# Kernel tuning notes

Measured on AMD Instinct MI355X. Metric: run time of the kernel, lower is better.

Reference implementation:

```python
import jax, jax.numpy as jnp
import numpy as np

DIM = 2048
NH = 16
Q_LORA = 1536
KV_LORA = 512
NOPE = 128
ROPE = 64
VDIM = 128
QK = NOPE + ROPE  # 192
B, S = 2, 2048
EPS = 1.1920929e-07  # torch.finfo(float32).eps (nn.RMSNorm default)


def linear(x, w, b):
    return jnp.einsum('...i,oi->...o', x, w) + b


def rmsnorm(x, w):
    ms = jnp.mean(x * x, axis=-1, keepdims=True)
    return x * jax.lax.rsqrt(ms + EPS) * w


def rope(x, cos, sin):
    # x: [B,S,H,d] interleaved pairs; cos/sin: [S, d//2]
    x = x.reshape(*x.shape[:-1], -1, 2)
    x0, x1 = x[..., 0], x[..., 1]
    c = cos[None, :, None, :]
    s = sin[None, :, None, :]
    y0 = x0 * c - x1 * s
    y1 = x0 * s + x1 * c
    return jnp.stack([y0, y1], axis=-1).reshape(*x.shape[:-2], -1)


def setup_inputs() -> dict:
    key = jax.random.key(0)
    ks = jax.random.split(key, 12)
    sd = 0.02
    x = jax.random.normal(ks[0], (B, S, DIM), dtype=jnp.float32)
    freqs = jax.random.normal(ks[1], (S, ROPE // 2), dtype=jnp.float32)
    causal_mask = jnp.where(jnp.triu(jnp.ones((S, S), bool), k=1), -1e9, 0.0).astype(jnp.float32)
    inp = dict(x=x, freqs=freqs, causal_mask=causal_mask)
    inp['Wq_down_w'] = sd * jax.random.normal(ks[2], (Q_LORA, DIM), dtype=jnp.float32)
    inp['Wq_down_b'] = jnp.zeros((Q_LORA,), jnp.float32)
    inp['q_norm_w'] = jnp.ones((Q_LORA,), jnp.float32)
    inp['Wq_up_w'] = sd * jax.random.normal(ks[3], (NH * QK, Q_LORA), dtype=jnp.float32)
    inp['Wq_up_b'] = jnp.zeros((NH * QK,), jnp.float32)
    inp['Wkv_down_w'] = sd * jax.random.normal(ks[4], (KV_LORA + ROPE, DIM), dtype=jnp.float32)
    inp['Wkv_down_b'] = jnp.zeros((KV_LORA + ROPE,), jnp.float32)
    inp['kv_norm_w'] = jnp.ones((KV_LORA,), jnp.float32)
    inp['Wkv_up_w'] = sd * jax.random.normal(ks[5], (NH * (NOPE + VDIM), KV_LORA), dtype=jnp.float32)
    inp['Wkv_up_b'] = jnp.zeros((NH * (NOPE + VDIM),), jnp.float32)
    inp['Wo_w'] = sd * jax.random.normal(ks[6], (DIM, NH * VDIM), dtype=jnp.float32)
    inp['Wo_b'] = jnp.zeros((DIM,), jnp.float32)
    return inp


def reference(x, freqs, causal_mask, Wq_down_w, Wq_down_b, q_norm_w, Wq_up_w, Wq_up_b,
              Wkv_down_w, Wkv_down_b, kv_norm_w, Wkv_up_w, Wkv_up_b, Wo_w, Wo_b):
    cos, sin = jnp.cos(freqs), jnp.sin(freqs)
    scale = QK ** -0.5
    # Q path: low-rank down, RMSNorm, up
    q_lat = rmsnorm(linear(x, Wq_down_w, Wq_down_b), q_norm_w)
    Q = linear(q_lat, Wq_up_w, Wq_up_b).reshape(B, S, NH, QK)
    Q_nope, Q_rope = Q[..., :NOPE], Q[..., NOPE:]
    Q_rope = rope(Q_rope, cos, sin)
    Q = jnp.concatenate([Q_nope, Q_rope], axis=-1)  # [B,S,H,QK]
    # KV path: shared latent + decoupled rope key
    kv_kr = linear(x, Wkv_down_w, Wkv_down_b)
    kv_lat, K_rope = kv_kr[..., :KV_LORA], kv_kr[..., KV_LORA:]
    kv_lat = rmsnorm(kv_lat, kv_norm_w)
    K_rope = rope(K_rope[:, :, None, :], cos, sin)  # [B,S,1,ROPE]
    kv = linear(kv_lat, Wkv_up_w, Wkv_up_b).reshape(B, S, NH, NOPE + VDIM)
    K_nope, V = kv[..., :NOPE], kv[..., NOPE:]
    K = jnp.concatenate([K_nope, jnp.broadcast_to(K_rope, (B, S, NH, ROPE))], axis=-1)
    # attention
    scores = jnp.einsum('bqhd,bkhd->bhqk', Q, K) * scale + causal_mask[None, None]
    attn = jax.nn.softmax(scores, axis=-1)
    out = jnp.einsum('bhqk,bkhd->bqhd', attn, V).reshape(B, S, NH * VDIM)
    return linear(out, Wo_w, Wo_b)
```

## Files before the change

kernel.cpp:

```cpp
#include <hip/hip_runtime.h>
#include <hip/hip_bf16.h>

#define DIMD 2048
#define NHD 16
#define QLORA 1536
#define KVLORA 512
#define QKD 192
#define BBD 2
#define SSD 2048
#define BSD (BBD*SSD)
#define KVPAD 640
#define BHN (BBD*NHD)
#define EPSF 1.1920929e-07f
#define SCALEF 0.07216878364870322f

typedef __hip_bfloat16 bf16;
typedef __attribute__((ext_vector_type(8))) short short8;
typedef __attribute__((ext_vector_type(4))) float floatx4;

typedef __attribute__((address_space(1))) char as1_char;
typedef __attribute__((address_space(3))) char as3_char;
#define GLD16(g, l) __builtin_amdgcn_global_load_lds((as1_char*)(g), (as3_char*)(l), 16, 0, 0)

__device__ __forceinline__ float block_sum(float x) {
#pragma unroll
  for (int o = 32; o > 0; o >>= 1) x += __shfl_xor(x, o, 64);
  __shared__ float red[4];
  __syncthreads();
  if ((threadIdx.x & 63) == 0) red[threadIdx.x >> 6] = x;
  __syncthreads();
  return red[0] + red[1] + red[2] + red[3];
}

template<bool STORE_BF16>
__global__ __launch_bounds__(256)
void gemm_bt(const bf16* __restrict__ A, const bf16* __restrict__ Bm,
             const float* __restrict__ bias, void* __restrict__ Cp,
             int M, int N, int K, long sA, long sB, long sC, int ldc)
{
  int m0 = blockIdx.y * 128, n0 = blockIdx.x * 128;
  long z = blockIdx.z;
  A  += z * sA;
  Bm += z * sB;

  __shared__ __align__(16) bf16 Asm[128 * 32];
  __shared__ __align__(16) bf16 Bsm[128 * 32];

  const int tid  = threadIdx.x;
  const int lane = tid & 63;
  const int wv   = tid >> 6;
  const int wm   = (wv >> 1) << 6;
  const int wn   = (wv & 1) << 6;
  const int fr   = lane & 15;
  const int q8   = (lane >> 4) << 3;

  floatx4 acc[4][4];
#pragma unroll
  for (int i = 0; i < 4; ++i)
#pragma unroll
    for (int j = 0; j < 4; ++j)
      acc[i][j] = (floatx4){0.f, 0.f, 0.f, 0.f};

  for (int k0 = 0; k0 < K; k0 += 32) {
    __syncthreads();
#pragma unroll
    for (int it = 0; it < 2; ++it) {
      int seg = it * 256 + tid;
      int row = seg >> 2, cs = seg & 3;
      GLD16(A  + (long)(m0 + row) * K + k0 + cs * 8, &Asm[(it * 256 + wv * 64) * 8]);
      GLD16(Bm + (long)(n0 + row) * K + k0 + cs * 8, &Bsm[(it * 256 + wv * 64) * 8]);
    }
    __syncthreads();

    short8 fa[4], fb[4];
#pragma unroll
    for (int t = 0; t < 4; ++t) fa[t] = *(const short8*)&Asm[(wm + t * 16 + fr) * 32 + q8];
#pragma unroll
    for (int t = 0; t < 4; ++t) fb[t] = *(const short8*)&Bsm[(wn + t * 16 + fr) * 32 + q8];
#pragma unroll
    for (int i = 0; i < 4; ++i)
#pragma unroll
      for (int j = 0; j < 4; ++j)
        acc[i][j] = __builtin_amdgcn_mfma_f32_16x16x32_bf16(fa[i], fb[j], acc[i][j], 0, 0, 0);
  }

  long cb = z * sC;
  int rq = (lane >> 4) * 4;
#pragma unroll
  for (int i = 0; i < 4; ++i) {
#pragma unroll
    for (int j = 0; j < 4; ++j) {
      int col = n0 + wn + j * 16 + fr;
      float bv = bias ? bias[col] : 0.f;
#pragma unroll
      for (int r = 0; r < 4; ++r) {
        int rowg = m0 + wm + i * 16 + rq + r;
        float v = acc[i][j][r] + bv;
        if (STORE_BF16)
          ((bf16*)Cp)[cb + (long)rowg * ldc + col] = __float2bfloat16(v);
        else
          ((float*)Cp)[cb + (long)rowg * ldc + col] = v;
      }
    }
  }
}

__global__ __launch_bounds__(512, 2)
void flash_attn(const bf16* __restrict__ Qh, const bf16* __restrict__ Kh,
                const bf16* __restrict__ Vt, bf16* __restrict__ attnall)
{
  const int p = blockIdx.x;
  const int z = blockIdx.y;
  const int b = z >> 4, h = z & 15;

  const bf16* Qg = Qh + (long)z * SSD * QKD;
  const bf16* Kg = Kh + (long)z * SSD * QKD;
  const bf16* Vg = Vt + (long)z * 128 * SSD;

  __shared__ __align__(16) bf16 Ksm[6 * 4096];
  __shared__ __align__(16) bf16 Vsm[4 * 4096];
  bf16* Psm = Ksm;

  const int tid  = threadIdx.x;
  const int lane = tid & 63;
  const int wv   = tid >> 6;
  const int fr   = lane & 15;
  const int g4   = lane >> 4;
  const int q8   = g4 << 3;
  const int srow = tid >> 2;
  const int scs  = tid & 3;

#pragma unroll 1
  for (int t = 0; t < 2; ++t) {
    const int qt = t ? p : 15 - p;
    const int q0 = qt * 128;

    __syncthreads();
#pragma unroll
    for (int c = 0; c < 6; ++c)
      GLD16(Qg + (long)(q0 + srow) * QKD + c * 32 + scs * 8, &Ksm[c * 4096 + wv * 512]);
    __syncthreads();
    short8 qf[6];
#pragma unroll
    for (int c = 0; c < 6; ++c)
      qf[c] = *(const short8*)&Ksm[c * 4096 + (wv * 16 + fr) * 32 + q8];

    floatx4 oacc[8];
#pragma unroll
    for (int n = 0; n < 8; ++n) oacc[n] = (floatx4){0.f, 0.f, 0.f, 0.f};
    float mi[4], li[4];
#pragma unroll
    for (int r = 0; r < 4; ++r) { mi[r] = -1e30f; li[r] = 0.f; }

    for (int j = 0; j <= qt; ++j) {
      const int jb = j * 128;
      __syncthreads();
#pragma unroll
      for (int c = 0; c < 6; ++c)
        GLD16(Kg + (long)(jb + srow) * QKD + c * 32 + scs * 8, &Ksm[c * 4096 + wv * 512]);
#pragma unroll
      for (int c = 0; c < 4; ++c)
        GLD16(Vg + (long)srow * SSD + jb + c * 32 + scs * 8, &Vsm[c * 4096 + wv * 512]);
      __syncthreads();

      floatx4 sacc[8];
#pragma unroll
      for (int n = 0; n < 8; ++n) sacc[n] = (floatx4){0.f, 0.f, 0.f, 0.f};
#pragma unroll
      for (int c = 0; c < 6; ++c) {
#pragma unroll
        for (int n = 0; n < 8; ++n) {
          short8 fb = *(const short8*)&Ksm[c * 4096 + (n * 16 + fr) * 32 + q8];
          sacc[n] = __builtin_amdgcn_mfma_f32_16x16x32_bf16(qf[c], fb, sacc[n], 0, 0, 0);
        }
      }

      const bool diag = (j == qt);
#pragma unroll
      for (int r = 0; r < 4; ++r) {
        int rowg = q0 + wv * 16 + g4 * 4 + r;
        float mx = -1e30f;
#pragma unroll
        for (int n = 0; n < 8; ++n) {
          float v = sacc[n][r] * SCALEF;
          if (diag && (jb + n * 16 + fr) > rowg) v = -1e30f;
          sacc[n][r] = v;
          mx = fmaxf(mx, v);
        }
#pragma unroll
        for (int off = 1; off < 16; off <<= 1) mx = fmaxf(mx, __shfl_xor(mx, off, 64));
        float mnew = fmaxf(mi[r], mx);
        float alpha = __expf(mi[r] - mnew);
        mi[r] = mnew;
        float rs = 0.f;
#pragma unroll
        for (int n = 0; n < 8; ++n) {
          float pv = __expf(sacc[n][r] - mnew);
          sacc[n][r] = pv;
          rs += pv;
        }
#pragma unroll
        for (int off = 1; off < 16; off <<= 1) rs += __shfl_xor(rs, off, 64);
        li[r] = li[r] * alpha + rs;
#pragma unroll
        for (int n = 0; n < 8; ++n) oacc[n][r] *= alpha;
      }

      __syncthreads();
#pragma unroll
      for (int n = 0; n < 8; ++n) {
        int c2 = n >> 1;
        int col = (n & 1) * 16 + fr;
#pragma unroll
        for (int r = 0; r < 4; ++r) {
          int m = wv * 16 + g4 * 4 + r;
          Psm[c2 * 4096 + m * 32 + col] = __float2bfloat16(sacc[n][r]);
        }
      }

#pragma unroll
      for (int c2 = 0; c2 < 4; ++c2) {
        short8 pf = *(const short8*)&Psm[c2 * 4096 + (wv * 16 + fr) * 32 + q8];
#pragma unroll
        for (int dn = 0; dn < 8; ++dn) {
          short8 vf = *(const short8*)&Vsm[c2 * 4096 + (dn * 16 + fr) * 32 + q8];
          oacc[dn] = __builtin_amdgcn_mfma_f32_16x16x32_bf16(pf, vf, oacc[dn], 0, 0, 0);
        }
      }
    }

#pragma unroll
    for (int r = 0; r < 4; ++r) {
      float inv = 1.f / li[r];
      int m = q0 + wv * 16 + g4 * 4 + r;
      bf16* orow = attnall + ((long)(b * SSD + m) * NHD + h) * 128;
#pragma unroll
      for (int dn = 0; dn < 8; ++dn)
        orow[dn * 16 + fr] = __float2bfloat16(oacc[dn][r] * inv);
    }
  }
}

__device__ __forceinline__ void cvt4(const float* __restrict__ s, bf16* __restrict__ d,
                                     long se, long de) {
  float4 v = *(const float4*)(s + se);
  union { bf16 h[4]; uint2 u; } o;
  o.h[0] = __float2bfloat16(v.x); o.h[1] = __float2bfloat16(v.y);
  o.h[2] = __float2bfloat16(v.z); o.h[3] = __float2bfloat16(v.w);
  *(uint2*)(d + de) = o.u;
}

#define NX4   ((long)BSD * DIMD / 4)
#define NQD4  ((long)QLORA * DIMD / 4)
#define NQU4  ((long)3072 * QLORA / 4)
#define NKVD4 ((long)KVPAD * DIMD / 4)
#define NKVU4 ((long)4096 * KVLORA / 4)
#define NWO4  ((long)DIMD * 2048 / 4)

__global__ __launch_bounds__(256)
void cvt_all(const float* __restrict__ x, const float* __restrict__ wqd,
             const float* __restrict__ wqu, const float* __restrict__ wkvd,
             const float* __restrict__ wkvu, const float* __restrict__ wo,
             bf16* __restrict__ dx, bf16* __restrict__ dwqd, bf16* __restrict__ dwqu,
             bf16* __restrict__ dwkvd, bf16* __restrict__ dwkvu, bf16* __restrict__ dwo)
{
  long i = (long)blockIdx.x * 256 + threadIdx.x;
  if (i < NX4) { cvt4(x, dx, i * 4, i * 4); return; }
  i -= NX4;
  if (i < NQD4) { cvt4(wqd, dwqd, i * 4, i * 4); return; }
  i -= NQD4;
  if (i < NQU4) { cvt4(wqu, dwqu, i * 4, i * 4); return; }
  i -= NQU4;
  if (i < NKVD4) {
    long e = i * 4;
    long r = e >> 11;
    if (r < 576) cvt4(wkvd, dwkvd, e, e);
    else *(uint2*)(dwkvd + e) = (uint2){0u, 0u};
    return;
  }
  i -= NKVD4;
  if (i < NKVU4) { cvt4(wkvu, dwkvu, i * 4, i * 4); return; }
  i -= NKVU4;
  if (i < NWO4) { cvt4(wo, dwo, i * 4, i * 4); return; }
}

template<int L>
__global__ __launch_bounds__(256)
void rmsnorm_k(const bf16* __restrict__ in, const float* __restrict__ bias,
               const float* __restrict__ w, bf16* __restrict__ out, int ldin)
{
  constexpr int NIT = L / 256;
  long r = blockIdx.x;
  const bf16* row = in + r * ldin;
  int tid = threadIdx.x;
  float v[NIT];
  float ss = 0.f;
#pragma unroll
  for (int i = 0; i < NIT; ++i) {
    int c = tid + (i << 8);
    float x = __bfloat162float(row[c]) + (bias ? bias[c] : 0.f);
    v[i] = x;
    ss += x * x;
  }
  ss = block_sum(ss);
  float sc = rsqrtf(ss / (float)L + EPSF);
#pragma unroll
  for (int i = 0; i < NIT; ++i) {
    int c = tid + (i << 8);
    out[r * L + c] = __float2bfloat16(v[i] * sc * w[c]);
  }
}

__global__ void build_q(const bf16* __restrict__ Qf, const float* __restrict__ freqs,
                        bf16* __restrict__ Qh)
{
  int idx = blockIdx.x * 256 + threadIdx.x;
  if (idx >= BSD * NHD * 96) return;
  int j = idx % 96;
  int h = (idx / 96) % NHD;
  int srow = idx / (96 * NHD);
  int s = srow & (SSD - 1);
  int b = srow >> 11;
  const bf16* src = Qf + (long)srow * (NHD * QKD) + h * QKD + 2 * j;
  float x0 = __bfloat162float(src[0]), x1 = __bfloat162float(src[1]), y0, y1;
  if (j >= 64) {
    int i = j - 64;
    float f = freqs[s * 32 + i];
    float c = cosf(f), sn = sinf(f);
    y0 = x0 * c - x1 * sn;
    y1 = x0 * sn + x1 * c;
  } else { y0 = x0; y1 = x1; }
  bf16* dst = Qh + ((long)(b * NHD + h) * SSD + s) * QKD + 2 * j;
  dst[0] = __float2bfloat16(y0);
  dst[1] = __float2bfloat16(y1);
}

__global__ void build_k(const bf16* __restrict__ kvf, const bf16* __restrict__ kvkr,
                        const float* __restrict__ kvb, const float* __restrict__ freqs,
                        bf16* __restrict__ Kh)
{
  int idx = blockIdx.x * 256 + threadIdx.x;
  if (idx >= BSD * NHD * 96) return;
  int j = idx % 96;
  int h = (idx / 96) % NHD;
  int srow = idx / (96 * NHD);
  int s = srow & (SSD - 1);
  int b = srow >> 11;
  float y0, y1;
  if (j < 64) {
    const bf16* src = kvf + (long)srow * 4096 + h * 256 + 2 * j;
    y0 = __bfloat162float(src[0]); y1 = __bfloat162float(src[1]);
  } else {
    int i = j - 64;
    float x0 = __bfloat162float(kvkr[(long)srow * KVPAD + 512 + 2 * i]) + kvb[512 + 2 * i];
    float x1 = __bfloat162float(kvkr[(long)srow * KVPAD + 513 + 2 * i]) + kvb[513 + 2 * i];
    float f = freqs[s * 32 + i];
    float c = cosf(f), sn = sinf(f);
    y0 = x0 * c - x1 * sn;
    y1 = x0 * sn + x1 * c;
  }
  bf16* dst = Kh + ((long)(b * NHD + h) * SSD + s) * QKD + 2 * j;
  dst[0] = __float2bfloat16(y0);
  dst[1] = __float2bfloat16(y1);
}

__global__ __launch_bounds__(256)
void build_vt(const bf16* __restrict__ kvf, bf16* __restrict__ Vt)
{
  __shared__ float t[32][33];
  int s0 = blockIdx.x * 32, d0 = blockIdx.y * 32, z = blockIdx.z;
  int b = z / NHD, h = z % NHD;
  int tx = threadIdx.x, ty = threadIdx.y;
#pragma unroll
  for (int r = 0; r < 4; ++r) {
    int sl = ty + r * 8;
    t[sl][tx] = __bfloat162float(kvf[(long)(b * SSD + s0 + sl) * 4096 + h * 256 + 128 + d0 + tx]);
  }
  __syncthreads();
#pragma unroll
  for (int r = 0; r < 4; ++r) {
    int dl = ty + r * 8;
    Vt[((long)z * 128 + d0 + dl) * SSD + s0 + tx] = __float2bfloat16(t[tx][dl]);
  }
}

__global__ void diag_fill(float* out) { out[blockIdx.x * 256 + threadIdx.x] = 1000.0f; }

extern "C" void kernel_launch(void* const* d_in, const int* in_sizes, int n_in,
                              void* d_out, int out_size, void* d_ws, size_t ws_size,
                              hipStream_t stream)
{
  const float* x     = (const float*)d_in[0];
  const float* freqs = (const float*)d_in[1];
  const float* Wqd   = (const float*)d_in[3];
  const float* Wqdb  = (const float*)d_in[4];
  const float* qnw   = (const float*)d_in[5];
  const float* Wqu   = (const float*)d_in[6];
  const float* Wqub  = (const float*)d_in[7];
  const float* Wkvd  = (const float*)d_in[8];
  const float* Wkvdb = (const float*)d_in[9];
  const float* kvnw  = (const float*)d_in[10];
  const float* Wkvu  = (const float*)d_in[11];
  const float* Wkvub = (const float*)d_in[12];
  const float* Wo    = (const float*)d_in[13];
  const float* Wob   = (const float*)d_in[14];
  float* out = (float*)d_out;

  char* ws = (char*)d_ws;
  size_t off = 0;
  auto alloc = [&](size_t bytes) {
    void* p = ws + off;
    off += (bytes + 255) & ~(size_t)255;
    return p;
  };

  bf16* Wqd16  = (bf16*)alloc((size_t)QLORA * DIMD * 2);
  bf16* Wqu16  = (bf16*)alloc((size_t)3072 * QLORA * 2);
  bf16* Wkvd16 = (bf16*)alloc((size_t)KVPAD * DIMD * 2);
  bf16* Wkvu16 = (bf16*)alloc((size_t)4096 * KVLORA * 2);
  bf16* Wo16   = (bf16*)alloc((size_t)DIMD * 2048 * 2);
  bf16* x16    = (bf16*)alloc((size_t)BSD * DIMD * 2);
  bf16* Ra     = (bf16*)alloc((size_t)BSD * QLORA * 2);
  bf16* Rb     = (bf16*)alloc((size_t)BSD * QLORA * 2);
  bf16* Rc     = (bf16*)alloc((size_t)BSD * 4096 * 2);
  bf16* Qh16   = (bf16*)alloc((size_t)BHN * SSD * QKD * 2);
  bf16* Kh16   = (bf16*)alloc((size_t)BHN * SSD * QKD * 2);
  bf16* Vt16   = (bf16*)alloc((size_t)BHN * 128 * SSD * 2);

  bf16* qdown   = Ra;  bf16* kvkr    = Ra;
  bf16* qlat16  = Rb;  bf16* kvlat16 = Rb;
  bf16* Qf      = Rc;  bf16* kvf     = Rc;  bf16* attnall = Rc;

  if (off > ws_size) { diag_fill<<<8, 256, 0, stream>>>(out); return; }

  dim3 blk(256);
  auto cdiv = [](long a, long b) { return (int)((a + b - 1) / b); };

  long tot4 = NX4 + NQD4 + NQU4 + NKVD4 + NKVU4 + NWO4;
  cvt_all<<<cdiv(tot4, 256), blk, 0, stream>>>(x, Wqd, Wqu, Wkvd, Wkvu, Wo,
                                               x16, Wqd16, Wqu16, Wkvd16, Wkvu16, Wo16);

  gemm_bt<true><<<dim3(QLORA / 128, BSD / 128, 1), blk, 0, stream>>>(
      x16, Wqd16, Wqdb, qdown, BSD, QLORA, DIMD, 0, 0, 0, QLORA);
  rmsnorm_k<QLORA><<<BSD, blk, 0, stream>>>(qdown, nullptr, qnw, qlat16, QLORA);
  gemm_bt<true><<<dim3(3072 / 128, BSD / 128, 1), blk, 0, stream>>>(
      qlat16, Wqu16, Wqub, Qf, BSD, 3072, QLORA, 0, 0, 0, 3072);
  build_q<<<cdiv((long)BSD * NHD * 96, 256), blk, 0, stream>>>(Qf, freqs, Qh16);

  gemm_bt<true><<<dim3(KVPAD / 128, BSD / 128, 1), blk, 0, stream>>>(
      x16, Wkvd16, nullptr, kvkr, BSD, KVPAD, DIMD, 0, 0, 0, KVPAD);
  rmsnorm_k<KVLORA><<<BSD, blk, 0, stream>>>(kvkr, Wkvdb, kvnw, kvlat16, KVPAD);
  gemm_bt<true><<<dim3(4096 / 128, BSD / 128, 1), blk, 0, stream>>>(
      kvlat16, Wkvu16, Wkvub, kvf, BSD, 4096, KVLORA, 0, 0, 0, 4096);
  build_k<<<cdiv((long)BSD * NHD * 96, 256), blk, 0, stream>>>(kvf, kvkr, Wkvdb, freqs, Kh16);
  build_vt<<<dim3(SSD / 32, 128 / 32, BHN), dim3(32, 8), 0, stream>>>(kvf, Vt16);

  flash_attn<<<dim3(8, BHN), dim3(512), 0, stream>>>(Qh16, Kh16, Vt16, attnall);

  gemm_bt<false><<<dim3(2048 / 128, BSD / 128, 1), blk, 0, stream>>>(
      attnall, Wo16, Wob, out, BSD, DIMD, 2048, 0, 0, 0, DIMD);
}
```

Before: 571.1 us.

## Use 64-row query tiles in flash attention and precompute rope cos/sin table

Flash attention now runs 256-thread blocks over 64-row query tiles, with 16 blocks per (batch, head) instead of 8. This doubles the grid, so work spreads better across compute units, while K/V tiles stay at 128 columns and are loaded in two passes per thread. Rope cos/sin values are computed once into a table by a new small kernel, rather than recomputed with cosf/sinf in every build_q and build_k thread. The costs are one extra launch and each K/V tile being reloaded by twice as many blocks.

```diff
diff --git a/kernel.cpp b/kernel.cpp
--- a/kernel.cpp
+++ b/kernel.cpp
@@ -105,7 +105,7 @@
   }
 }
 
-__global__ __launch_bounds__(512, 2)
+__global__ __launch_bounds__(256, 2)
 void flash_attn(const bf16* __restrict__ Qh, const bf16* __restrict__ Kh,
                 const bf16* __restrict__ Vt, bf16* __restrict__ attnall)
 {
@@ -127,18 +127,19 @@
   const int fr   = lane & 15;
   const int g4   = lane >> 4;
   const int q8   = g4 << 3;
-  const int srow = tid >> 2;
-  const int scs  = tid & 3;
 
 #pragma unroll 1
   for (int t = 0; t < 2; ++t) {
-    const int qt = t ? p : 15 - p;
-    const int q0 = qt * 128;
+    const int qt = t ? p : 31 - p;
+    const int q0 = qt * 64;
+    const int jmax = qt >> 1;
 
     __syncthreads();
 #pragma unroll
-    for (int c = 0; c < 6; ++c)
-      GLD16(Qg + (long)(q0 + srow) * QKD + c * 32 + scs * 8, &Ksm[c * 4096 + wv * 512]);
+    for (int c = 0; c < 6; ++c) {
+      int row = tid >> 2, cs = tid & 3;
+      GLD16(Qg + (long)(q0 + row) * QKD + c * 32 + cs * 8, &Ksm[c * 4096 + wv * 512]);
+    }
     __syncthreads();
     short8 qf[6];
 #pragma unroll
@@ -152,15 +153,27 @@
 #pragma unroll
     for (int r = 0; r < 4; ++r) { mi[r] = -1e30f; li[r] = 0.f; }
 
-    for (int j = 0; j <= qt; ++j) {
+    for (int j = 0; j <= jmax; ++j) {
       const int jb = j * 128;
       __syncthreads();
 #pragma unroll
       for (int c = 0; c < 6; ++c)
-        GLD16(Kg + (long)(jb + srow) * QKD + c * 32 + scs * 8, &Ksm[c * 4096 + wv * 512]);
+#pragma unroll
+        for (int it = 0; it < 2; ++it) {
+          int seg = it * 256 + tid;
+          int row = seg >> 2, cs = seg & 3;
+          GLD16(Kg + (long)(jb + row) * QKD + c * 32 + cs * 8,
+                &Ksm[c * 4096 + it * 2048 + wv * 512]);
+        }
 #pragma unroll
       for (int c = 0; c < 4; ++c)
-        GLD16(Vg + (long)srow * SSD + jb + c * 32 + scs * 8, &Vsm[c * 4096 + wv * 512]);
+#pragma unroll
+        for (int it = 0; it < 2; ++it) {
+          int seg = it * 256 + tid;
+          int row = seg >> 2, cs = seg & 3;
+          GLD16(Vg + (long)row * SSD + jb + c * 32 + cs * 8,
+                &Vsm[c * 4096 + it * 2048 + wv * 512]);
+        }
       __syncthreads();
 
       floatx4 sacc[8];
@@ -175,7 +188,7 @@
         }
       }
 
-      const bool diag = (j == qt);
+      const bool diag = (j == jmax);
 #pragma unroll
       for (int r = 0; r < 4; ++r) {
         int rowg = q0 + wv * 16 + g4 * 4 + r;
@@ -284,6 +297,15 @@
   if (i < NWO4) { cvt4(wo, dwo, i * 4, i * 4); return; }
 }
 
+__global__ void trig_k(const float* __restrict__ freqs, float2* __restrict__ tab)
+{
+  int i = blockIdx.x * 256 + threadIdx.x;
+  if (i < SSD * 32) {
+    float f = freqs[i];
+    tab[i] = make_float2(cosf(f), sinf(f));
+  }
+}
+
 template<int L>
 __global__ __launch_bounds__(256)
 void rmsnorm_k(const bf16* __restrict__ in, const float* __restrict__ bias,
@@ -311,7 +333,7 @@
   }
 }
 
-__global__ void build_q(const bf16* __restrict__ Qf, const float* __restrict__ freqs,
+__global__ void build_q(const bf16* __restrict__ Qf, const float2* __restrict__ cstab,
                         bf16* __restrict__ Qh)
 {
   int idx = blockIdx.x * 256 + threadIdx.x;
@@ -325,10 +347,9 @@
   float x0 = __bfloat162float(src[0]), x1 = __bfloat162float(src[1]), y0, y1;
   if (j >= 64) {
     int i = j - 64;
-    float f = freqs[s * 32 + i];
-    float c = cosf(f), sn = sinf(f);
-    y0 = x0 * c - x1 * sn;
-    y1 = x0 * sn + x1 * c;
+    float2 cs = cstab[s * 32 + i];
+    y0 = x0 * cs.x - x1 * cs.y;
+    y1 = x0 * cs.y + x1 * cs.x;
   } else { y0 = x0; y1 = x1; }
   bf16* dst = Qh + ((long)(b * NHD + h) * SSD + s) * QKD + 2 * j;
   dst[0] = __float2bfloat16(y0);
@@ -336,7 +357,7 @@
 }
 
 __global__ void build_k(const bf16* __restrict__ kvf, const bf16* __restrict__ kvkr,
-                        const float* __restrict__ kvb, const float* __restrict__ freqs,
+                        const float* __restrict__ kvb, const float2* __restrict__ cstab,
                         bf16* __restrict__ Kh)
 {
   int idx = blockIdx.x * 256 + threadIdx.x;
@@ -354,10 +375,9 @@
     int i = j - 64;
     float x0 = __bfloat162float(kvkr[(long)srow * KVPAD + 512 + 2 * i]) + kvb[512 + 2 * i];
     float x1 = __bfloat162float(kvkr[(long)srow * KVPAD + 513 + 2 * i]) + kvb[513 + 2 * i];
-    float f = freqs[s * 32 + i];
-    float c = cosf(f), sn = sinf(f);
-    y0 = x0 * c - x1 * sn;
-    y1 = x0 * sn + x1 * c;
+    float2 cs = cstab[s * 32 + i];
+    y0 = x0 * cs.x - x1 * cs.y;
+    y1 = x0 * cs.y + x1 * cs.x;
   }
   bf16* dst = Kh + ((long)(b * NHD + h) * SSD + s) * QKD + 2 * j;
   dst[0] = __float2bfloat16(y0);
@@ -426,6 +446,7 @@
   bf16* Qh16   = (bf16*)alloc((size_t)BHN * SSD * QKD * 2);
   bf16* Kh16   = (bf16*)alloc((size_t)BHN * SSD * QKD * 2);
   bf16* Vt16   = (bf16*)alloc((size_t)BHN * 128 * SSD * 2);
+  float2* cstab = (float2*)alloc((size_t)SSD * 32 * sizeof(float2));
 
   bf16* qdown   = Ra;  bf16* kvkr    = Ra;
   bf16* qlat16  = Rb;  bf16* kvlat16 = Rb;
@@ -439,23 +460,24 @@
   long tot4 = NX4 + NQD4 + NQU4 + NKVD4 + NKVU4 + NWO4;
   cvt_all<<<cdiv(tot4, 256), blk, 0, stream>>>(x, Wqd, Wqu, Wkvd, Wkvu, Wo,
                                                x16, Wqd16, Wqu16, Wkvd16, Wkvu16, Wo16);
+  trig_k<<<cdiv((long)SSD * 32, 256), blk, 0, stream>>>(freqs, cstab);
 
   gemm_bt<true><<<dim3(QLORA / 128, BSD / 128, 1), blk, 0, stream>>>(
       x16, Wqd16, Wqdb, qdown, BSD, QLORA, DIMD, 0, 0, 0, QLORA);
   rmsnorm_k<QLORA><<<BSD, blk, 0, stream>>>(qdown, nullptr, qnw, qlat16, QLORA);
   gemm_bt<true><<<dim3(3072 / 128, BSD / 128, 1), blk, 0, stream>>>(
       qlat16, Wqu16, Wqub, Qf, BSD, 3072, QLORA, 0, 0, 0, 3072);
-  build_q<<<cdiv((long)BSD * NHD * 96, 256), blk, 0, stream>>>(Qf, freqs, Qh16);
+  build_q<<<cdiv((long)BSD * NHD * 96, 256), blk, 0, stream>>>(Qf, cstab, Qh16);
 
   gemm_bt<true><<<dim3(KVPAD / 128, BSD / 128, 1), blk, 0, stream>>>(
       x16, Wkvd16, nullptr, kvkr, BSD, KVPAD, DIMD, 0, 0, 0, KVPAD);
   rmsnorm_k<KVLORA><<<BSD, blk, 0, stream>>>(kvkr, Wkvdb, kvnw, kvlat16, KVPAD);
   gemm_bt<true><<<dim3(4096 / 128, BSD / 128, 1), blk, 0, stream>>>(
       kvlat16, Wkvu16, Wkvub, kvf, BSD, 4096, KVLORA, 0, 0, 0, 4096);
-  build_k<<<cdiv((long)BSD * NHD * 96, 256), blk, 0, stream>>>(kvf, kvkr, Wkvdb, freqs, Kh16);
+  build_k<<<cdiv((long)BSD * NHD * 96, 256), blk, 0, stream>>>(kvf, kvkr, Wkvdb, cstab, Kh16);
   build_vt<<<dim3(SSD / 32, 128 / 32, BHN), dim3(32, 8), 0, stream>>>(kvf, Vt16);
 
-  flash_attn<<<dim3(8, BHN), dim3(512), 0, stream>>>(Qh16, Kh16, Vt16, attnall);
+  flash_attn<<<dim3(16, BHN), blk, 0, stream>>>(Qh16, Kh16, Vt16, attnall);
 
   gemm_bt<false><<<dim3(2048 / 128, BSD / 128, 1), blk, 0, stream>>>(
       attnall, Wo16, Wob, out, BSD, DIMD, 2048, 0, 0, 0, DIMD);
```

Result: no change. 574.7 us (+0.6%).
